# Kernel optimization log

Hardware: AMD Instinct MI355X
Metric: run time of the kernel (lower is better)

Reference implementation:

```python
import math
import jax, jax.numpy as jnp
import numpy as np

B = 512
E = 512
C = 70722
M_MARGIN = 0.4
H = 0.333
S = 64.0
T_ALPHA = 1.0
EPS = 1e-3


def setup_inputs() -> dict:
    key = jax.random.key(0)
    k1, k2, k3, k4 = jax.random.split(key, 4)
    embbedings = jax.random.normal(k1, (B, E), dtype=jnp.float32)
    embbedings = embbedings / jnp.linalg.norm(embbedings, axis=1, keepdims=True)
    # feature norms typically ~[10, 30] for face models
    norms = 10.0 + 20.0 * jax.random.uniform(k2, (B, 1), dtype=jnp.float32)
    label = jax.random.randint(k3, (B,), 0, C, dtype=jnp.int64)
    kernel = jax.random.normal(k4, (E, C), dtype=jnp.float32)
    batch_mean = jnp.ones((C,), dtype=jnp.float32) * 20.0
    batch_std = jnp.asarray(10.0, dtype=jnp.float32)
    return {"embbedings": embbedings, "norms": norms, "label": label,
            "kernel": kernel, "batch_mean": batch_mean, "batch_std": batch_std}


def reference(embbedings, norms, label, kernel, batch_mean, batch_std):
    # column-wise l2-normalize the class weight matrix [E, C]
    kernel_norm = kernel / jnp.linalg.norm(kernel, axis=0, keepdims=True)
    cosine = jnp.clip(embbedings @ kernel_norm, -1.0 + EPS, 1.0 - EPS)  # [B, C]
    safe_norms = jnp.clip(norms, 1e-3, 100.0)  # [B, 1]

    # ---- running-stat update (torch.no_grad block) ----
    sn = jax.lax.stop_gradient(safe_norms[:, 0])  # [B]
    sums = jnp.zeros((C,), dtype=sn.dtype).at[label].add(sn)
    counts = jnp.zeros((C,), dtype=sn.dtype).at[label].add(1.0)
    group_mean = sums / jnp.maximum(counts, 1.0)  # per-class batch mean of norms
    new_mean = jnp.where(counts > 0,
                         group_mean * T_ALPHA + (1.0 - T_ALPHA) * batch_mean,
                         batch_mean)
    std = jnp.std(sn, ddof=1)  # torch.std is unbiased
    new_std = std * T_ALPHA + (1.0 - T_ALPHA) * batch_std

    # ---- adaptive margin ----
    margin_scaler = (safe_norms - new_mean[label][:, None]) / (new_std + EPS)
    margin_scaler = jnp.clip(margin_scaler * H, -1.0, 1.0)  # [B, 1]

    oh = jax.nn.one_hot(label, C, dtype=cosine.dtype)  # [B, C]
    g_angular = -M_MARGIN * margin_scaler               # [B, 1]
    theta = jnp.arccos(cosine)
    theta_m = jnp.clip(theta + oh * g_angular, EPS, math.pi - EPS)
    g_add = M_MARGIN + M_MARGIN * margin_scaler         # [B, 1]
    out = (jnp.cos(theta_m) - oh * g_add) * S
    return out
```

## Files before the change

kernel.cpp:

```cpp
#include <hip/hip_runtime.h>
#include <hip/hip_bf16.h>
#include <cstdint>
#include <cstddef>
#include <math.h>

#define B_SZ 512
#define E_SZ 512
#define C_SZ 70722
#define BN 64
#define NBLK 1106
#define M_MARGIN 0.4f
#define H_CONST 0.333f
#define S_CONST 64.0f
#define EPS_F 1e-3f
#define PI_F 3.14159265358979323846f

typedef __attribute__((ext_vector_type(8))) short short8;
typedef __attribute__((ext_vector_type(4))) float f32x4;


__device__ __forceinline__ unsigned short f2bf(float x) {
  __hip_bfloat16 h = __float2bfloat16(x);
  unsigned short u;
  __builtin_memcpy(&u, &h, 2);
  return u;
}

__device__ __forceinline__ void gload_lds16(const void* g, void* l) {
  __builtin_amdgcn_global_load_lds(
      (const __attribute__((address_space(1))) unsigned int*)g,
      (__attribute__((address_space(3))) unsigned int*)l, 16, 0, 0);
}

__global__ void k_stats(const float* __restrict__ norms, const int* __restrict__ label,
                        float* __restrict__ ga, float* __restrict__ gadd) {
  __shared__ float sn[B_SZ];
  __shared__ int lab[B_SZ];
  __shared__ float redA[8], redB[8];
  __shared__ float sh_std;

  int t = threadIdx.x;
  float v = norms[t];
  v = fminf(fmaxf(v, 1e-3f), 100.0f);
  sn[t] = v;
  lab[t] = label[t];

  float s1 = v, s2 = v * v;
  #pragma unroll
  for (int o = 32; o > 0; o >>= 1) {
    s1 += __shfl_down(s1, o);
    s2 += __shfl_down(s2, o);
  }
  if ((t & 63) == 0) { redA[t >> 6] = s1; redB[t >> 6] = s2; }
  __syncthreads();
  if (t == 0) {
    float a = 0.f, b = 0.f;
    #pragma unroll
    for (int i = 0; i < 8; ++i) { a += redA[i]; b += redB[i]; }
    float mean = a / (float)B_SZ;
    float var = (b - (float)B_SZ * mean * mean) / (float)(B_SZ - 1);
    sh_std = sqrtf(fmaxf(var, 0.f));
  }
  __syncthreads();
  float stdv = sh_std;

  int myl = lab[t];
  float s = 0.f, cnt = 0.f;
  for (int j = 0; j < B_SZ; ++j) {
    bool m = (lab[j] == myl);
    s += m ? sn[j] : 0.f;
    cnt += m ? 1.f : 0.f;
  }
  float gm = s / fmaxf(cnt, 1.f);
  float ms = (v - gm) / (stdv + EPS_F) * H_CONST;
  ms = fminf(fmaxf(ms, -1.f), 1.f);
  ga[t] = -M_MARGIN * ms;
  gadd[t] = M_MARGIN + M_MARGIN * ms;
}

__global__ void k_cvtA(const float* __restrict__ emb, unsigned short* __restrict__ abf) {
  int i = (blockIdx.x * 256 + threadIdx.x) * 4;
  float4 f = *(const float4*)(emb + i);
  unsigned short u0 = f2bf(f.x), u1 = f2bf(f.y), u2 = f2bf(f.z), u3 = f2bf(f.w);
  unsigned long long pk = (unsigned long long)u0 | ((unsigned long long)u1 << 16) |
                          ((unsigned long long)u2 << 32) | ((unsigned long long)u3 << 48);
  *(unsigned long long*)(abf + i) = pk;
}

__launch_bounds__(512, 4)
__global__ void k_gemm_full(const unsigned short* __restrict__ Abf,
                            const float* __restrict__ Kmat,
                            const int* __restrict__ label,
                            const float* __restrict__ ga,
                            const float* __restrict__ gadd,
                            float* __restrict__ out) {
  __shared__ __align__(16) unsigned short As[512 * 32];
  __shared__ __align__(16) unsigned short Bs[2][BN * 32];
  __shared__ float red[8][BN];
  __shared__ float invn_s[BN];
  __shared__ int lab_s[512];

  const int tid = threadIdx.x;
  const int w = tid >> 6;
  const int lane = tid & 63;
  const int q = lane >> 4;
  const int l15 = lane & 15;

  const int c0 = blockIdx.x * BN;
  const bool edge = (c0 + BN > C_SZ);

  lab_s[tid] = label[tid];

  const int r_loc = tid >> 4;
  const int bcol = c0 + (l15 << 2);
  const int cT = (l15 << 2) + q;
  const int sigT = l15 & 3;
  char* const bwr = (char*)&Bs[0][0] + cT * 64 + (((w >> 1) ^ sigT) & 3) * 16 + ((w & 1) << 3);

  const int arow_l = lane >> 2;
  const int acg = (lane & 3) ^ q;
  char* const adst = (char*)As + (w * 64) * 64;

  const int sfrag = l15 >> 2;
  int offA[4], offB[4];
  #pragma unroll
  for (int m = 0; m < 4; ++m) {
    int row = w * 64 + m * 16 + l15;
    offA[m] = row * 64 + ((q ^ sfrag) & 3) * 16;
  }
  #pragma unroll
  for (int n = 0; n < 4; ++n) {
    int c = n * 16 + l15;
    offB[n] = c * 64 + ((q ^ sfrag) & 3) * 16;
  }

  f32x4 acc[4][4];
  #pragma unroll
  for (int m = 0; m < 4; ++m)
    #pragma unroll
    for (int n = 0; n < 4; ++n)
      acc[m][n] = f32x4{0.f, 0.f, 0.f, 0.f};

  float ss0 = 0.f, ss1 = 0.f, ss2 = 0.f, ss3 = 0.f;

#define BLOAD(bv, kb)                                                        \
  {                                                                          \
    const float* src = Kmat + (size_t)((kb) + r_loc) * C_SZ + bcol;          \
    if (!edge) {                                                             \
      bv = *(const float4*)src;                                              \
    } else {                                                                 \
      bv.x = (bcol + 0 < C_SZ) ? src[0] : 0.f;                               \
      bv.y = (bcol + 1 < C_SZ) ? src[1] : 0.f;                               \
      bv.z = (bcol + 2 < C_SZ) ? src[2] : 0.f;                               \
      bv.w = (bcol + 3 < C_SZ) ? src[3] : 0.f;                               \
    }                                                                        \
  }

#define BXPOSE_WRITE(bv, buf)                                                \
  {                                                                          \
    ss0 += bv.x * bv.x; ss1 += bv.y * bv.y;                                  \
    ss2 += bv.z * bv.z; ss3 += bv.w * bv.w;                                  \
    bool h32 = (lane & 32) != 0;                                             \
    float t2 = h32 ? bv.x : bv.z;                                            \
    float t3 = h32 ? bv.y : bv.w;                                            \
    float x2 = __shfl_xor(t2, 32);                                           \
    float x3 = __shfl_xor(t3, 32);                                           \
    float u0 = h32 ? x2 : bv.x;                                              \
    float u1 = h32 ? x3 : bv.y;                                              \
    float u2 = h32 ? bv.z : x2;                                              \
    float u3 = h32 ? bv.w : x3;                                              \
    bool h16 = (lane & 16) != 0;                                             \
    float s0 = h16 ? u0 : u1;                                                \
    float s1 = h16 ? u2 : u3;                                                \
    float z0 = __shfl_xor(s0, 16);                                           \
    float z1 = __shfl_xor(s1, 16);                                           \
    float y0 = h16 ? z0 : u0;                                                \
    float y1 = h16 ? u1 : z0;                                                \
    float y2 = h16 ? z1 : u2;                                                \
    float y3 = h16 ? u3 : z1;                                                \
    unsigned long long pk = (unsigned long long)f2bf(y0) |                   \
                            ((unsigned long long)f2bf(y1) << 16) |           \
                            ((unsigned long long)f2bf(y2) << 32) |           \
                            ((unsigned long long)f2bf(y3) << 48);            \
    *(unsigned long long*)(bwr + (buf) * 4096) = pk;                         \
  }

#define ASTAGE(kb)                                                           \
  {                                                                          \
    _Pragma("unroll")                                                        \
    for (int rr = 0; rr < 4; ++rr) {                                         \
      int r = w * 64 + rr * 16 + arow_l;                                     \
      gload_lds16(Abf + (size_t)r * 512 + (kb) + acg * 8, adst + rr * 1024); \
    }                                                                        \
  }

  ASTAGE(0)
  {
    float4 bv;
    BLOAD(bv, 0)
    BXPOSE_WRITE(bv, 0)
  }
  __syncthreads();

  for (int kt = 0; kt < 16; ++kt) {
    const int cur = kt & 1;

    float4 bv;
    if (kt < 15) BLOAD(bv, (kt + 1) * 32)

    short8 a[4], b[4];
    const char* pB = (const char*)&Bs[0][0] + cur * 4096;
    #pragma unroll
    for (int m = 0; m < 4; ++m) a[m] = *(const short8*)((const char*)As + offA[m]);
    #pragma unroll
    for (int n = 0; n < 4; ++n) b[n] = *(const short8*)(pB + offB[n]);

    #pragma unroll
    for (int m = 0; m < 4; ++m)
      #pragma unroll
      for (int n = 0; n < 4; ++n)
        acc[m][n] = __builtin_amdgcn_mfma_f32_16x16x32_bf16(a[m], b[n], acc[m][n], 0, 0, 0);

    __syncthreads();

    if (kt < 15) {
      ASTAGE((kt + 1) * 32)
      BXPOSE_WRITE(bv, cur ^ 1)
    }
    __syncthreads();
  }
#undef BLOAD
#undef BXPOSE_WRITE
#undef ASTAGE

  ss0 += __shfl_xor(ss0, 16); ss0 += __shfl_xor(ss0, 32);
  ss1 += __shfl_xor(ss1, 16); ss1 += __shfl_xor(ss1, 32);
  ss2 += __shfl_xor(ss2, 16); ss2 += __shfl_xor(ss2, 32);
  ss3 += __shfl_xor(ss3, 16); ss3 += __shfl_xor(ss3, 32);
  if (lane < 16) {
    red[w][l15 * 4 + 0] = ss0;
    red[w][l15 * 4 + 1] = ss1;
    red[w][l15 * 4 + 2] = ss2;
    red[w][l15 * 4 + 3] = ss3;
  }
  __syncthreads();
  if (tid < BN) {
    float s = 0.f;
    #pragma unroll
    for (int r = 0; r < 8; ++r) s += red[r][tid];
    invn_s[tid] = (s > 0.f) ? rsqrtf(s) : 0.f;
  }
  __syncthreads();

  float invc[4];
  #pragma unroll
  for (int n = 0; n < 4; ++n) invc[n] = invn_s[n * 16 + l15];

  #pragma unroll
  for (int m = 0; m < 4; ++m) {
    int grow0 = w * 64 + m * 16 + q * 4;
    #pragma unroll
    for (int n = 0; n < 4; ++n) {
      int gc = c0 + n * 16 + l15;
      if (gc >= C_SZ) continue;
      #pragma unroll
      for (int r = 0; r < 4; ++r) {
        int grow = grow0 + r;
        float v = acc[m][n][r] * invc[n];
        v = fminf(fmaxf(v, -1.f + EPS_F), 1.f - EPS_F);
        float res = v * S_CONST;
        if (gc == lab_s[grow]) {
          float th = acosf(v) + ga[grow];
          th = fminf(fmaxf(th, EPS_F), PI_F - EPS_F);
          res = (cosf(th) - gadd[grow]) * S_CONST;
        }
        out[(size_t)grow * C_SZ + gc] = res;
      }
    }
  }
}

extern "C" void kernel_launch(void* const* d_in, const int* in_sizes, int n_in,
                              void* d_out, int out_size, void* d_ws, size_t ws_size,
                              hipStream_t stream) {
  const float* emb   = (const float*)d_in[0];
  const float* norms = (const float*)d_in[1];
  const int*   label = (const int*)d_in[2];
  const float* kmat  = (const float*)d_in[3];
  float* out = (float*)d_out;

  char* ws = (char*)d_ws;
  float* ga   = (float*)ws;
  float* gadd = (float*)(ws + 2048);
  unsigned short* abf = (unsigned short*)(ws + 4096);

  k_stats<<<1, 512, 0, stream>>>(norms, label, ga, gadd);
  k_cvtA<<<256, 256, 0, stream>>>(emb, abf);
  k_gemm_full<<<NBLK, 512, 0, stream>>>(abf, kmat, label, ga, gadd, out);
}
```

Before: 150.4 us.

## Deepen GEMM K-tile to 64 with register-prefetched B and manual barrier schedule

Doubles the K step per stage from 32 to 64, which halves the barrier count to 8 iterations. It adds a two-slot register prefetch of the fp32 kernel tiles two stages ahead, with explicit waitcnt and sched_barrier control, and changes the LDS swizzle to an XOR pattern for 128-byte rows. It also caches ga and gadd in LDS for the epilogue. The larger LDS footprint and register use lower the launch-bounds occupancy from 4 to 2 blocks per CU, which risks less latency hiding.

New measurement: 165.4 us. +10.0%, slower.

```diff
diff --git a/kernel.cpp b/kernel.cpp
--- a/kernel.cpp
+++ b/kernel.cpp
@@ -32,6 +32,29 @@
       (__attribute__((address_space(3))) unsigned int*)l, 16, 0, 0);
 }
 
+__device__ __forceinline__ f32x4 xpose4(float4 v, int lane) {
+  bool h32 = (lane & 32) != 0;
+  float t2 = h32 ? v.x : v.z;
+  float t3 = h32 ? v.y : v.w;
+  float x2 = __shfl_xor(t2, 32);
+  float x3 = __shfl_xor(t3, 32);
+  float u0 = h32 ? x2 : v.x;
+  float u1 = h32 ? x3 : v.y;
+  float u2 = h32 ? v.z : x2;
+  float u3 = h32 ? v.w : x3;
+  bool h16 = (lane & 16) != 0;
+  float s0 = h16 ? u0 : u1;
+  float s1 = h16 ? u2 : u3;
+  float z0 = __shfl_xor(s0, 16);
+  float z1 = __shfl_xor(s1, 16);
+  f32x4 y;
+  y[0] = h16 ? z0 : u0;
+  y[1] = h16 ? u1 : z0;
+  y[2] = h16 ? z1 : u2;
+  y[3] = h16 ? u3 : z1;
+  return y;
+}
+
 __global__ void k_stats(const float* __restrict__ norms, const int* __restrict__ label,
                         float* __restrict__ ga, float* __restrict__ gadd) {
   __shared__ float sn[B_SZ];
@@ -87,51 +110,53 @@
   *(unsigned long long*)(abf + i) = pk;
 }
 
-__launch_bounds__(512, 4)
+__launch_bounds__(512, 2)
 __global__ void k_gemm_full(const unsigned short* __restrict__ Abf,
                             const float* __restrict__ Kmat,
                             const int* __restrict__ label,
                             const float* __restrict__ ga,
                             const float* __restrict__ gadd,
                             float* __restrict__ out) {
-  __shared__ __align__(16) unsigned short As[512 * 32];
-  __shared__ __align__(16) unsigned short Bs[2][BN * 32];
-  __shared__ float red[8][BN];
-  __shared__ float invn_s[BN];
+  __shared__ __align__(16) unsigned short As[512 * 64];
+  __shared__ __align__(16) unsigned short Bs[2][64 * 64];
+  __shared__ float red[8][64];
+  __shared__ float invn_s[64];
   __shared__ int lab_s[512];
+  __shared__ float ga_s[512], gadd_s[512];
 
   const int tid = threadIdx.x;
   const int w = tid >> 6;
   const int lane = tid & 63;
   const int q = lane >> 4;
   const int l15 = lane & 15;
-
   const int c0 = blockIdx.x * BN;
   const bool edge = (c0 + BN > C_SZ);
 
   lab_s[tid] = label[tid];
-
-  const int r_loc = tid >> 4;
-  const int bcol = c0 + (l15 << 2);
-  const int cT = (l15 << 2) + q;
-  const int sigT = l15 & 3;
-  char* const bwr = (char*)&Bs[0][0] + cT * 64 + (((w >> 1) ^ sigT) & 3) * 16 + ((w & 1) << 3);
-
-  const int arow_l = lane >> 2;
-  const int acg = (lane & 3) ^ q;
-  char* const adst = (char*)As + (w * 64) * 64;
-
-  const int sfrag = l15 >> 2;
+  ga_s[tid] = ga[tid];
+  gadd_s[tid] = gadd[tid];
+
+  const int ar = lane >> 3;
+  const int ac = lane & 7;
+  char* const adst = (char*)As + (w * 64) * 128;
+
+  const float* const bsrc = Kmat + (size_t)(w * 8 + q * 2) * C_SZ + c0 + l15 * 4;
+  const int cT = l15 * 4 + q;
+  const int swzT = (cT & 7) ^ ((cT >> 2) & 7);
+  char* const bdst = (char*)&Bs[0][0] + cT * 128 + ((w ^ swzT) << 4);
+
   int offA[4], offB[4];
   #pragma unroll
   for (int m = 0; m < 4; ++m) {
     int row = w * 64 + m * 16 + l15;
-    offA[m] = row * 64 + ((q ^ sfrag) & 3) * 16;
+    int swz = (row & 7) ^ ((row >> 2) & 7);
+    offA[m] = row * 128 + ((q ^ swz) << 4);
   }
   #pragma unroll
   for (int n = 0; n < 4; ++n) {
     int c = n * 16 + l15;
-    offB[n] = c * 64 + ((q ^ sfrag) & 3) * 16;
+    int swz = (c & 7) ^ ((c >> 2) & 7);
+    offB[n] = c * 128 + ((q ^ swz) << 4);
   }
 
   f32x4 acc[4][4];
@@ -141,108 +166,130 @@
     for (int n = 0; n < 4; ++n)
       acc[m][n] = f32x4{0.f, 0.f, 0.f, 0.f};
 
-  float ss0 = 0.f, ss1 = 0.f, ss2 = 0.f, ss3 = 0.f;
-
-#define BLOAD(bv, kb)                                                        \
-  {                                                                          \
-    const float* src = Kmat + (size_t)((kb) + r_loc) * C_SZ + bcol;          \
-    if (!edge) {                                                             \
-      bv = *(const float4*)src;                                              \
-    } else {                                                                 \
-      bv.x = (bcol + 0 < C_SZ) ? src[0] : 0.f;                               \
-      bv.y = (bcol + 1 < C_SZ) ? src[1] : 0.f;                               \
-      bv.z = (bcol + 2 < C_SZ) ? src[2] : 0.f;                               \
-      bv.w = (bcol + 3 < C_SZ) ? src[3] : 0.f;                               \
-    }                                                                        \
-  }
-
-#define BXPOSE_WRITE(bv, buf)                                                \
-  {                                                                          \
-    ss0 += bv.x * bv.x; ss1 += bv.y * bv.y;                                  \
-    ss2 += bv.z * bv.z; ss3 += bv.w * bv.w;                                  \
-    bool h32 = (lane & 32) != 0;                                             \
-    float t2 = h32 ? bv.x : bv.z;                                            \
-    float t3 = h32 ? bv.y : bv.w;                                            \
-    float x2 = __shfl_xor(t2, 32);                                           \
-    float x3 = __shfl_xor(t3, 32);                                           \
-    float u0 = h32 ? x2 : bv.x;                                              \
-    float u1 = h32 ? x3 : bv.y;                                              \
-    float u2 = h32 ? bv.z : x2;                                              \
-    float u3 = h32 ? bv.w : x3;                                              \
-    bool h16 = (lane & 16) != 0;                                             \
-    float s0 = h16 ? u0 : u1;                                                \
-    float s1 = h16 ? u2 : u3;                                                \
-    float z0 = __shfl_xor(s0, 16);                                           \
-    float z1 = __shfl_xor(s1, 16);                                           \
-    float y0 = h16 ? z0 : u0;                                                \
-    float y1 = h16 ? u1 : z0;                                                \
-    float y2 = h16 ? z1 : u2;                                                \
-    float y3 = h16 ? u3 : z1;                                                \
-    unsigned long long pk = (unsigned long long)f2bf(y0) |                   \
-                            ((unsigned long long)f2bf(y1) << 16) |           \
-                            ((unsigned long long)f2bf(y2) << 32) |           \
-                            ((unsigned long long)f2bf(y3) << 48);            \
-    *(unsigned long long*)(bwr + (buf) * 4096) = pk;                         \
-  }
-
-#define ASTAGE(kb)                                                           \
-  {                                                                          \
-    _Pragma("unroll")                                                        \
-    for (int rr = 0; rr < 4; ++rr) {                                         \
-      int r = w * 64 + rr * 16 + arow_l;                                     \
-      gload_lds16(Abf + (size_t)r * 512 + (kb) + acg * 8, adst + rr * 1024); \
-    }                                                                        \
+  float ss = 0.f;
+  float4 bv[2][2];
+
+#define ASTAGE(KB)                                                          \
+  {                                                                         \
+    _Pragma("unroll")                                                       \
+    for (int rr = 0; rr < 8; ++rr) {                                        \
+      int r = w * 64 + rr * 8 + ar;                                         \
+      int s = ac ^ ((r & 7) ^ ((r >> 2) & 7));                              \
+      gload_lds16(Abf + (size_t)r * 512 + (KB) + s * 8, adst + rr * 1024);  \
+    }                                                                       \
+  }
+
+#define BLOADP(SLOT, KB)                                                    \
+  {                                                                         \
+    const float* s0 = bsrc + (size_t)(KB) * C_SZ;                           \
+    if (!edge) {                                                            \
+      bv[SLOT][0] = *(const float4*)s0;                                     \
+      bv[SLOT][1] = *(const float4*)(s0 + C_SZ);                            \
+    } else {                                                                \
+      float* p0 = (float*)&bv[SLOT][0];                                     \
+      float* p1 = (float*)&bv[SLOT][1];                                     \
+      _Pragma("unroll")                                                     \
+      for (int j = 0; j < 4; ++j) {                                         \
+        bool ok = (c0 + l15 * 4 + j) < C_SZ;                                \
+        p0[j] = ok ? s0[j] : 0.f;                                           \
+        p1[j] = ok ? s0[(size_t)C_SZ + j] : 0.f;                            \
+      }                                                                     \
+    }                                                                       \
+  }
+
+#define XW(SLOT, BUF)                                                       \
+  {                                                                         \
+    f32x4 te = xpose4(bv[SLOT][0], lane);          \
+    f32x4 to = xpose4(bv[SLOT][1], lane);          \
+    ss += te[0] * te[0] + to[0] * to[0];                                    \
+    ss += te[1] * te[1] + to[1] * to[1];                                    \
+    ss += te[2] * te[2] + to[2] * to[2];                                    \
+    ss += te[3] * te[3] + to[3] * to[3];                                    \
+    uint4 pk;                                                               \
+    pk.x = (unsigned)f2bf(te[0]) | ((unsigned)f2bf(to[0]) << 16);           \
+    pk.y = (unsigned)f2bf(te[1]) | ((unsigned)f2bf(to[1]) << 16);           \
+    pk.z = (unsigned)f2bf(te[2]) | ((unsigned)f2bf(to[2]) << 16);           \
+    pk.w = (unsigned)f2bf(te[3]) | ((unsigned)f2bf(to[3]) << 16);           \
+    *(uint4*)(bdst + (BUF) * 8192) = pk;                                    \
+  }
+
+#define COMPUTE(BUF)                                                        \
+  {                                                                         \
+    const char* pA = (const char*)As;                                       \
+    const char* pB = (const char*)&Bs[BUF][0];                              \
+    short8 a0[4], b0[4];                                                    \
+    _Pragma("unroll")                                                       \
+    for (int m = 0; m < 4; ++m) a0[m] = *(const short8*)(pA + offA[m]);     \
+    _Pragma("unroll")                                                       \
+    for (int n = 0; n < 4; ++n) b0[n] = *(const short8*)(pB + offB[n]);     \
+    _Pragma("unroll")                                                       \
+    for (int m = 0; m < 4; ++m)                                             \
+      _Pragma("unroll")                                                     \
+      for (int n = 0; n < 4; ++n)                                           \
+        acc[m][n] = __builtin_amdgcn_mfma_f32_16x16x32_bf16(a0[m], b0[n], acc[m][n], 0, 0, 0); \
+    _Pragma("unroll")                                                       \
+    for (int m = 0; m < 4; ++m) a0[m] = *(const short8*)(pA + (offA[m] ^ 64)); \
+    _Pragma("unroll")                                                       \
+    for (int n = 0; n < 4; ++n) b0[n] = *(const short8*)(pB + (offB[n] ^ 64)); \
+    _Pragma("unroll")                                                       \
+    for (int m = 0; m < 4; ++m)                                             \
+      _Pragma("unroll")                                                     \
+      for (int n = 0; n < 4; ++n)                                           \
+        acc[m][n] = __builtin_amdgcn_mfma_f32_16x16x32_bf16(a0[m], b0[n], acc[m][n], 0, 0, 0); \
   }
 
   ASTAGE(0)
-  {
-    float4 bv;
-    BLOAD(bv, 0)
-    BXPOSE_WRITE(bv, 0)
-  }
-  __syncthreads();
-
-  for (int kt = 0; kt < 16; ++kt) {
-    const int cur = kt & 1;
-
-    float4 bv;
-    if (kt < 15) BLOAD(bv, (kt + 1) * 32)
-
-    short8 a[4], b[4];
-    const char* pB = (const char*)&Bs[0][0] + cur * 4096;
-    #pragma unroll
-    for (int m = 0; m < 4; ++m) a[m] = *(const short8*)((const char*)As + offA[m]);
-    #pragma unroll
-    for (int n = 0; n < 4; ++n) b[n] = *(const short8*)(pB + offB[n]);
-
-    #pragma unroll
-    for (int m = 0; m < 4; ++m)
-      #pragma unroll
-      for (int n = 0; n < 4; ++n)
-        acc[m][n] = __builtin_amdgcn_mfma_f32_16x16x32_bf16(a[m], b[n], acc[m][n], 0, 0, 0);
-
-    __syncthreads();
-
-    if (kt < 15) {
-      ASTAGE((kt + 1) * 32)
-      BXPOSE_WRITE(bv, cur ^ 1)
-    }
-    __syncthreads();
-  }
-#undef BLOAD
-#undef BXPOSE_WRITE
+  __builtin_amdgcn_sched_barrier(0);
+  BLOADP(0, 0)
+  BLOADP(1, 64)
+  XW(0, 0)
+  asm volatile("s_waitcnt vmcnt(2) lgkmcnt(0)" ::: "memory");
+  __builtin_amdgcn_sched_barrier(0);
+  __builtin_amdgcn_s_barrier();
+  __builtin_amdgcn_sched_barrier(0);
+
+#define STEP_MID(KT)                                                        \
+  COMPUTE((KT) & 1)                                                         \
+  __builtin_amdgcn_sched_barrier(0);                                        \
+  __builtin_amdgcn_s_barrier();        \
+  __builtin_amdgcn_sched_barrier(0);                                        \
+  ASTAGE(((KT) + 1) * 64)                        \
+  __builtin_amdgcn_sched_barrier(0);     \
+  BLOADP((KT) & 1, ((KT) + 2) * 64)                                         \
+  XW(((KT) + 1) & 1, ((KT) + 1) & 1)                                        \
+  asm volatile("s_waitcnt vmcnt(2) lgkmcnt(0)" ::: "memory");               \
+  __builtin_amdgcn_sched_barrier(0);                                        \
+  __builtin_amdgcn_s_barrier();                                             \
+  __builtin_amdgcn_sched_barrier(0);
+
+  STEP_MID(0)
+  STEP_MID(1)
+  STEP_MID(2)
+  STEP_MID(3)
+  STEP_MID(4)
+  STEP_MID(5)
+
+  COMPUTE(0)
+  __builtin_amdgcn_sched_barrier(0);
+  __builtin_amdgcn_s_barrier();
+  __builtin_amdgcn_sched_barrier(0);
+  ASTAGE(7 * 64)
+  XW(1, 1)
+  asm volatile("s_waitcnt vmcnt(0) lgkmcnt(0)" ::: "memory");
+  __builtin_amdgcn_sched_barrier(0);
+  __builtin_amdgcn_s_barrier();
+  __builtin_amdgcn_sched_barrier(0);
+
+  COMPUTE(1)
+
+#undef STEP_MID
+#undef COMPUTE
+#undef XW
+#undef BLOADP
 #undef ASTAGE
 
-  ss0 += __shfl_xor(ss0, 16); ss0 += __shfl_xor(ss0, 32);
-  ss1 += __shfl_xor(ss1, 16); ss1 += __shfl_xor(ss1, 32);
-  ss2 += __shfl_xor(ss2, 16); ss2 += __shfl_xor(ss2, 32);
-  ss3 += __shfl_xor(ss3, 16); ss3 += __shfl_xor(ss3, 32);
-  if (lane < 16) {
-    red[w][l15 * 4 + 0] = ss0;
-    red[w][l15 * 4 + 1] = ss1;
-    red[w][l15 * 4 + 2] = ss2;
-    red[w][l15 * 4 + 3] = ss3;
-  }
+  __syncthreads();
+  red[w][cT] = ss;
   __syncthreads();
   if (tid < BN) {
     float s = 0.f;
@@ -270,9 +317,9 @@
         v = fminf(fmaxf(v, -1.f + EPS_F), 1.f - EPS_F);
         float res = v * S_CONST;
         if (gc == lab_s[grow]) {
-          float th = acosf(v) + ga[grow];
+          float th = acosf(v) + ga_s[grow];
           th = fminf(fmaxf(th, EPS_F), PI_F - EPS_F);
-          res = (cosf(th) - gadd[grow]) * S_CONST;
+          res = (cosf(th) - gadd_s[grow]) * S_CONST;
         }
         out[(size_t)grow * C_SZ + gc] = res;
       }
```
